# Performance work log

Measured on AMD Instinct MI355X. Metric: run time of the kernel, lower is better.

Reference implementation:

```python
import jax, jax.numpy as jnp
import numpy as np

NEG = jnp.float32(-9e15)
SLOPE = 0.2  # LeakyReLU negative slope used in LocalAggregator


def setup_inputs() -> dict:
    key = jax.random.key(0)
    k1, k2, k3, k4, k5, k6, k7 = jax.random.split(key, 7)
    B, N, D, V = 32, 200, 100, 50000
    stdv = 1.0 / np.sqrt(D)
    inputs = jax.random.randint(k1, (B, N), 0, V)
    adj = jax.random.randint(k2, (B, N, N), 0, 5).astype(jnp.int32)
    mask_item = jnp.ones((B, N), dtype=jnp.int32)
    emb = jax.random.uniform(k3, (V, D), jnp.float32, -stdv, stdv)
    a0 = jax.random.uniform(k4, (D, 1), jnp.float32, -stdv, stdv)
    a1 = jax.random.uniform(k5, (D, 1), jnp.float32, -stdv, stdv)
    a2 = jax.random.uniform(k6, (D, 1), jnp.float32, -stdv, stdv)
    a3 = jax.random.uniform(k7, (D, 1), jnp.float32, -stdv, stdv)
    return {"inputs": inputs, "adj": adj, "mask_item": mask_item,
            "emb": emb, "a0": a0, "a1": a1, "a2": a2, "a3": a3}


def reference(inputs, adj, mask_item, emb, a0, a1, a2, a3):
    # h: [B, N, D] session item embeddings
    h = emb[inputs]
    # e_k[b,i,j] = leaky_relu(sum_d h[b,i,d]*h[b,j,d]*a_k[d])
    # (equivalent to the original (h_i * h_j) @ a_k without the BxNxNxD blowup)
    def edge_score(a):
        s = jnp.einsum('bid,bjd->bij', h * a[:, 0][None, None, :], h)
        return jax.nn.leaky_relu(s, SLOPE)
    e0, e1, e2, e3 = edge_score(a0), edge_score(a1), edge_score(a2), edge_score(a3)
    alpha = jnp.where(adj == 1, e0, NEG)
    alpha = jnp.where(adj == 2, e1, alpha)
    alpha = jnp.where(adj == 3, e2, alpha)
    alpha = jnp.where(adj == 4, e3, alpha)
    alpha = jax.nn.softmax(alpha, axis=-1)  # [B, N, N]
    # weighted aggregation over neighbors; dropout_local is inactive in eval
    return jnp.einsum('bij,bjd->bid', alpha, h)
```

## Files before the change

### kernel.cpp

```cpp
#include <hip/hip_runtime.h>
#include <math.h>

#define NEGV  (-9e15f)
#define SLOPE 0.2f

typedef __fp16 f16;
typedef __fp16 f16x4 __attribute__((ext_vector_type(4)));
typedef __fp16 f16x8 __attribute__((ext_vector_type(8)));
typedef float  f32x4 __attribute__((ext_vector_type(4)));

#define ZERO8 {(f16)0.f,(f16)0.f,(f16)0.f,(f16)0.f,(f16)0.f,(f16)0.f,(f16)0.f,(f16)0.f}

__global__ __launch_bounds__(256, 2) void gat_v11_kernel(
    const int*   __restrict__ inputs,
    const int*   __restrict__ adj,
    const float* __restrict__ emb,
    const float* __restrict__ a0, const float* __restrict__ a1,
    const float* __restrict__ a2, const float* __restrict__ a3,
    float*       __restrict__ out)
{
    const int b    = blockIdx.x / 13;
    const int i0   = (blockIdx.x % 13) * 16;
    const int tid  = threadIdx.x;
    const int wave = tid >> 6, lane = tid & 63;
    const int lj   = lane & 15, quad = lane >> 4, rbase = quad * 4;

    __shared__ f16   HF[200][104];
    __shared__ f16   ST[200][24];
    __shared__ int   sidx[200];
    __shared__ float reds[16][4];

    int kvv[4][4];
    #pragma unroll
    for (int jt = 0; jt < 4; ++jt) {
        const int j = (wave + 4 * jt) * 16 + lj;
        #pragma unroll
        for (int reg = 0; reg < 4; ++reg) {
            const int gi = i0 + rbase + reg;
            kvv[jt][reg] = (j < 200 && gi < 200)
                         ? adj[(size_t)(b * 200 + gi) * 200 + j] : 0;
        }
    }

    for (int t = tid; t < 200; t += 256) sidx[t] = inputs[b * 200 + t];
    __syncthreads();

    const float* aks[4] = {a0, a1, a2, a3};
    const int irow = i0 + lj;
    const float* hp = emb + (size_t)sidx[(irow < 200) ? irow : 199] * 100;
    f16x8 afr[4][4];
    #pragma unroll
    for (int ks = 0; ks < 4; ++ks) {
        const int base = ks * 32 + quad * 8;
        const bool full = (base <= 88), part = (base == 96);
        float4 hx = {0.f,0.f,0.f,0.f}, hy = {0.f,0.f,0.f,0.f};
        if (full)      { hx = *(const float4*)(hp + base); hy = *(const float4*)(hp + base + 4); }
        else if (part) { hx = *(const float4*)(hp + 96); }
        #pragma unroll
        for (int kk = 0; kk < 4; ++kk) {
            f16x8 o = ZERO8;
            if (full) {
                const float4 ax = *(const float4*)(aks[kk] + base);
                const float4 ay = *(const float4*)(aks[kk] + base + 4);
                o[0]=(f16)(hx.x*ax.x); o[1]=(f16)(hx.y*ax.y);
                o[2]=(f16)(hx.z*ax.z); o[3]=(f16)(hx.w*ax.w);
                o[4]=(f16)(hy.x*ay.x); o[5]=(f16)(hy.y*ay.y);
                o[6]=(f16)(hy.z*ay.z); o[7]=(f16)(hy.w*ay.w);
            } else if (part) {
                const float4 ax = *(const float4*)(aks[kk] + 96);
                o[0]=(f16)(hx.x*ax.x); o[1]=(f16)(hx.y*ax.y);
                o[2]=(f16)(hx.z*ax.z); o[3]=(f16)(hx.w*ax.w);
            }
            afr[kk][ks] = o;
        }
    }

    if (tid < 200) {
        const float4* src = (const float4*)(emb + (size_t)sidx[tid] * 100);
        f16x8* dst = (f16x8*)&HF[tid][0];
        #pragma unroll
        for (int c = 0; c < 12; ++c) {
            const float4 x = src[2*c], y = src[2*c+1];
            f16x8 o;
            o[0]=(f16)x.x; o[1]=(f16)x.y; o[2]=(f16)x.z; o[3]=(f16)x.w;
            o[4]=(f16)y.x; o[5]=(f16)y.y; o[6]=(f16)y.z; o[7]=(f16)y.w;
            dst[c] = o;
        }
        const float4 x = src[24];
        f16x8 o = ZERO8;
        o[0]=(f16)x.x; o[1]=(f16)x.y; o[2]=(f16)x.z; o[3]=(f16)x.w;
        dst[12] = o;
    }
    __syncthreads();

    float sel[4][4];
    #pragma unroll
    for (int jt = 0; jt < 4; ++jt) {
        const int j  = (wave + 4*jt)*16 + lj;
        const int jr = (j < 200) ? j : 199;
        const f16x8 b0 = *(const f16x8*)&HF[jr][     quad*8];
        const f16x8 b1 = *(const f16x8*)&HF[jr][32 + quad*8];
        const f16x8 b2 = *(const f16x8*)&HF[jr][64 + quad*8];
        const f16x8 b3 = *(const f16x8*)&HF[jr][96];
        f32x4 acck[4];
        #pragma unroll
        for (int kk = 0; kk < 4; ++kk) {
            f32x4 c = {0.f,0.f,0.f,0.f};
            c = __builtin_amdgcn_mfma_f32_16x16x32_f16(afr[kk][0], b0, c, 0,0,0);
            c = __builtin_amdgcn_mfma_f32_16x16x32_f16(afr[kk][1], b1, c, 0,0,0);
            c = __builtin_amdgcn_mfma_f32_16x16x32_f16(afr[kk][2], b2, c, 0,0,0);
            c = __builtin_amdgcn_mfma_f32_16x16x32_f16(afr[kk][3], b3, c, 0,0,0);
            acck[kk] = c;
        }
        #pragma unroll
        for (int reg = 0; reg < 4; ++reg) {
            const int k = kvv[jt][reg];
            float s = NEGV;
            if (k >= 1 && k <= 4) {
                const float v = (k==1)?acck[0][reg]:(k==2)?acck[1][reg]
                              :(k==3)?acck[2][reg]:acck[3][reg];
                s = (v >= 0.f) ? v : SLOPE * v;
            }
            sel[jt][reg] = s;
        }
    }

    float e[4][4], lsum[4];
    #pragma unroll
    for (int reg = 0; reg < 4; ++reg) lsum[reg] = 0.f;
    #pragma unroll
    for (int jt = 0; jt < 4; ++jt)
        #pragma unroll
        for (int reg = 0; reg < 4; ++reg) {
            e[jt][reg] = __expf(sel[jt][reg]);
            lsum[reg] += e[jt][reg];
        }
    #pragma unroll
    for (int reg = 0; reg < 4; ++reg) {
        float s = lsum[reg];
        #pragma unroll
        for (int off = 1; off <= 8; off <<= 1) s += __shfl_xor(s, off, 16);
        if (lj == 0) reds[rbase + reg][wave] = s;
    }
    __syncthreads();
    float inv[4];
    #pragma unroll
    for (int reg = 0; reg < 4; ++reg) {
        const float* rr = reds[rbase + reg];
        inv[reg] = 1.0f / (rr[0] + rr[1] + rr[2] + rr[3]);
    }
    #pragma unroll
    for (int jt = 0; jt < 4; ++jt) {
        const int j = (wave + 4*jt)*16 + lj;
        if (j < 200) {
            f16x4 w;
            #pragma unroll
            for (int reg = 0; reg < 4; ++reg)
                w[reg] = (f16)(e[jt][reg] * inv[reg]);
            *(f16x4*)&ST[j][rbase] = w;
        }
    }
    __syncthreads();

    const int ig = tid & 7;
    const int dq = tid >> 3;
    f32x4 o[16];
    #pragma unroll
    for (int i = 0; i < 16; ++i) o[i] = (f32x4){0.f,0.f,0.f,0.f};
    if (dq < 25) {
        for (int jj = 0; jj < 25; ++jj) {
            const int j = ig * 25 + jj;
            const f16x8 w0 = *(const f16x8*)&ST[j][0];
            const f16x8 w1 = *(const f16x8*)&ST[j][8];
            const f16x4 hv = *(const f16x4*)&HF[j][dq * 4];
            const float h0 = (float)hv[0], h1 = (float)hv[1],
                        h2 = (float)hv[2], h3 = (float)hv[3];
            #pragma unroll
            for (int i = 0; i < 8; ++i) {
                const float w = (float)w0[i];
                o[i][0] += w * h0; o[i][1] += w * h1;
                o[i][2] += w * h2; o[i][3] += w * h3;
            }
            #pragma unroll
            for (int i = 0; i < 8; ++i) {
                const float w = (float)w1[i];
                o[8+i][0] += w * h0; o[8+i][1] += w * h1;
                o[8+i][2] += w * h2; o[8+i][3] += w * h3;
            }
        }
    }
    #pragma unroll
    for (int i = 0; i < 16; ++i)
        #pragma unroll
        for (int c = 0; c < 4; ++c)
            #pragma unroll
            for (int off = 1; off <= 4; off <<= 1)
                o[i][c] += __shfl_xor(o[i][c], off, 8);
    if (dq < 25) {
        #pragma unroll
        for (int ii = 0; ii < 2; ++ii) {
            const int i  = ig * 2 + ii;
            const int gi = i0 + i;
            if (gi < 200)
                ((f32x4*)out)[(size_t)(b * 200 + gi) * 25 + dq] = o[i];
        }
    }
}

extern "C" void kernel_launch(void* const* d_in, const int* in_sizes, int n_in,
                              void* d_out, int out_size, void* d_ws, size_t ws_size,
                              hipStream_t stream) {
    const int*   inputs = (const int*)  d_in[0];
    const int*   adj    = (const int*)  d_in[1];
    const float* emb    = (const float*)d_in[3];
    const float* a0     = (const float*)d_in[4];
    const float* a1     = (const float*)d_in[5];
    const float* a2     = (const float*)d_in[6];
    const float* a3     = (const float*)d_in[7];
    float*       out    = (float*)d_out;

    gat_v11_kernel<<<dim3(32 * 13), dim3(256), 0, stream>>>(inputs, adj, emb, a0, a1, a2, a3, out);
}
```

Baseline: 107.0 us.

## Pre-pack gathered embeddings to fp16 workspace in a separate kernel

Adds a pack kernel that gathers each session's embedding rows and converts them once to padded fp16 in workspace. The main kernel then copies its batch's fp16 rows into shared memory with coalesced vector loads, instead of each of the 13 blocks per batch re-gathering and re-converting fp32 rows. This cuts redundant global gather traffic and conversion work, at the cost of a second kernel launch and a workspace round trip. The A fragments are now built from fp16-rounded h instead of fp32 h, which slightly changes precision.

```diff
diff --git a/kernel.cpp b/kernel.cpp
--- a/kernel.cpp
+++ b/kernel.cpp
@@ -11,10 +11,31 @@
 
 #define ZERO8 {(f16)0.f,(f16)0.f,(f16)0.f,(f16)0.f,(f16)0.f,(f16)0.f,(f16)0.f,(f16)0.f}
 
-__global__ __launch_bounds__(256, 2) void gat_v11_kernel(
+__global__ __launch_bounds__(256) void pack_kernel(
     const int*   __restrict__ inputs,
+    const float* __restrict__ emb,
+    f16*         __restrict__ hw)
+{
+    const int t = blockIdx.x * 256 + threadIdx.x;
+    if (t >= 6400 * 13) return;
+    const int r = t / 13, c = t % 13;
+    const float* src = emb + (size_t)inputs[r] * 100 + c * 8;
+    f16x8 o = ZERO8;
+    if (c < 12) {
+        const float4 x = *(const float4*)src;
+        const float4 y = *(const float4*)(src + 4);
+        o[0]=(f16)x.x; o[1]=(f16)x.y; o[2]=(f16)x.z; o[3]=(f16)x.w;
+        o[4]=(f16)y.x; o[5]=(f16)y.y; o[6]=(f16)y.z; o[7]=(f16)y.w;
+    } else {
+        const float4 x = *(const float4*)src;
+        o[0]=(f16)x.x; o[1]=(f16)x.y; o[2]=(f16)x.z; o[3]=(f16)x.w;
+    }
+    *(f16x8*)(hw + (size_t)r * 104 + c * 8) = o;
+}
+
+__global__ __launch_bounds__(256, 2) void gat_v12_kernel(
     const int*   __restrict__ adj,
-    const float* __restrict__ emb,
+    const f16*   __restrict__ hw,
     const float* __restrict__ a0, const float* __restrict__ a1,
     const float* __restrict__ a2, const float* __restrict__ a3,
     float*       __restrict__ out)
@@ -27,7 +48,6 @@
 
     __shared__ f16   HF[200][104];
     __shared__ f16   ST[200][24];
-    __shared__ int   sidx[200];
     __shared__ float reds[16][4];
 
     int kvv[4][4];
@@ -42,54 +62,47 @@
         }
     }
 
-    for (int t = tid; t < 200; t += 256) sidx[t] = inputs[b * 200 + t];
-    __syncthreads();
-
     const float* aks[4] = {a0, a1, a2, a3};
     const int irow = i0 + lj;
-    const float* hp = emb + (size_t)sidx[(irow < 200) ? irow : 199] * 100;
+    const f16* hp16 = hw + (size_t)(b * 200 + ((irow < 200) ? irow : 199)) * 104;
     f16x8 afr[4][4];
     #pragma unroll
     for (int ks = 0; ks < 4; ++ks) {
         const int base = ks * 32 + quad * 8;
         const bool full = (base <= 88), part = (base == 96);
-        float4 hx = {0.f,0.f,0.f,0.f}, hy = {0.f,0.f,0.f,0.f};
-        if (full)      { hx = *(const float4*)(hp + base); hy = *(const float4*)(hp + base + 4); }
-        else if (part) { hx = *(const float4*)(hp + 96); }
-        #pragma unroll
-        for (int kk = 0; kk < 4; ++kk) {
-            f16x8 o = ZERO8;
-            if (full) {
+        #pragma unroll
+        for (int kk = 0; kk < 4; ++kk) afr[kk][ks] = (f16x8)ZERO8;
+        if (full) {
+            const f16x8 hx = *(const f16x8*)(hp16 + base);
+            #pragma unroll
+            for (int kk = 0; kk < 4; ++kk) {
                 const float4 ax = *(const float4*)(aks[kk] + base);
                 const float4 ay = *(const float4*)(aks[kk] + base + 4);
-                o[0]=(f16)(hx.x*ax.x); o[1]=(f16)(hx.y*ax.y);
-                o[2]=(f16)(hx.z*ax.z); o[3]=(f16)(hx.w*ax.w);
-                o[4]=(f16)(hy.x*ay.x); o[5]=(f16)(hy.y*ay.y);
-                o[6]=(f16)(hy.z*ay.z); o[7]=(f16)(hy.w*ay.w);
-            } else if (part) {
+                f16x8 o;
+                o[0]=(f16)((float)hx[0]*ax.x); o[1]=(f16)((float)hx[1]*ax.y);
+                o[2]=(f16)((float)hx[2]*ax.z); o[3]=(f16)((float)hx[3]*ax.w);
+                o[4]=(f16)((float)hx[4]*ay.x); o[5]=(f16)((float)hx[5]*ay.y);
+                o[6]=(f16)((float)hx[6]*ay.z); o[7]=(f16)((float)hx[7]*ay.w);
+                afr[kk][ks] = o;
+            }
+        } else if (part) {
+            const f16x8 hx = *(const f16x8*)(hp16 + 96);
+            #pragma unroll
+            for (int kk = 0; kk < 4; ++kk) {
                 const float4 ax = *(const float4*)(aks[kk] + 96);
-                o[0]=(f16)(hx.x*ax.x); o[1]=(f16)(hx.y*ax.y);
-                o[2]=(f16)(hx.z*ax.z); o[3]=(f16)(hx.w*ax.w);
-            }
-            afr[kk][ks] = o;
-        }
-    }
-
-    if (tid < 200) {
-        const float4* src = (const float4*)(emb + (size_t)sidx[tid] * 100);
-        f16x8* dst = (f16x8*)&HF[tid][0];
-        #pragma unroll
-        for (int c = 0; c < 12; ++c) {
-            const float4 x = src[2*c], y = src[2*c+1];
-            f16x8 o;
-            o[0]=(f16)x.x; o[1]=(f16)x.y; o[2]=(f16)x.z; o[3]=(f16)x.w;
-            o[4]=(f16)y.x; o[5]=(f16)y.y; o[6]=(f16)y.z; o[7]=(f16)y.w;
-            dst[c] = o;
-        }
-        const float4 x = src[24];
-        f16x8 o = ZERO8;
-        o[0]=(f16)x.x; o[1]=(f16)x.y; o[2]=(f16)x.z; o[3]=(f16)x.w;
-        dst[12] = o;
+                f16x8 o = ZERO8;
+                o[0]=(f16)((float)hx[0]*ax.x); o[1]=(f16)((float)hx[1]*ax.y);
+                o[2]=(f16)((float)hx[2]*ax.z); o[3]=(f16)((float)hx[3]*ax.w);
+                afr[kk][ks] = o;
+            }
+        }
+    }
+
+    {
+        const f16x8* src = (const f16x8*)(hw + (size_t)b * 200 * 104);
+        f16x8* dst = (f16x8*)&HF[0][0];
+        #pragma unroll
+        for (int t = tid; t < 200 * 13; t += 256) dst[t] = src[t];
     }
     __syncthreads();
 
@@ -218,6 +231,8 @@
     const float* a2     = (const float*)d_in[6];
     const float* a3     = (const float*)d_in[7];
     float*       out    = (float*)d_out;
-
-    gat_v11_kernel<<<dim3(32 * 13), dim3(256), 0, stream>>>(inputs, adj, emb, a0, a1, a2, a3, out);
+    f16*         hw     = (f16*)d_ws;
+
+    pack_kernel  <<<dim3(325),     dim3(256), 0, stream>>>(inputs, emb, hw);
+    gat_v12_kernel<<<dim3(32 * 13), dim3(256), 0, stream>>>(adj, hw, a0, a1, a2, a3, out);
 }
```

Measured after the change: 110.1 us. 2.9% more time.

## Compute aggregation stage with MFMA using transposed attention weights in LDS

Applied to the files above, without the earlier changes.

Replaces the scalar FMA aggregation (alpha @ H) with 16x16x32 f16 MFMA instructions. Attention weights are now stored row-major per query row (STi[16][232], zero-padded) so they load directly as A fragments. H columns are gathered element-wise from LDS as B fragments. HF row stride changes to 108 to reduce bank conflicts, which needs split f16x4 loads and stores. The intent is to remove the large scalar FMA loop and the shuffle reduction, at the cost of strided 2-byte LDS gathers and fewer active waves in the second column tile.

```diff
diff --git a/kernel.cpp b/kernel.cpp
--- a/kernel.cpp
+++ b/kernel.cpp
@@ -9,9 +9,19 @@
 typedef __fp16 f16x8 __attribute__((ext_vector_type(8)));
 typedef float  f32x4 __attribute__((ext_vector_type(4)));
 
+#define ZERO4 {(f16)0.f,(f16)0.f,(f16)0.f,(f16)0.f}
 #define ZERO8 {(f16)0.f,(f16)0.f,(f16)0.f,(f16)0.f,(f16)0.f,(f16)0.f,(f16)0.f,(f16)0.f}
 
-__global__ __launch_bounds__(256, 2) void gat_v11_kernel(
+__device__ __forceinline__ f16x8 ld8(const f16* p) {
+    const f16x4 a = *(const f16x4*)p;
+    const f16x4 c = *(const f16x4*)(p + 4);
+    f16x8 r;
+    r[0]=a[0]; r[1]=a[1]; r[2]=a[2]; r[3]=a[3];
+    r[4]=c[0]; r[5]=c[1]; r[6]=c[2]; r[7]=c[3];
+    return r;
+}
+
+__global__ __launch_bounds__(256, 2) void gat_v15_kernel(
     const int*   __restrict__ inputs,
     const int*   __restrict__ adj,
     const float* __restrict__ emb,
@@ -25,8 +35,8 @@
     const int wave = tid >> 6, lane = tid & 63;
     const int lj   = lane & 15, quad = lane >> 4, rbase = quad * 4;
 
-    __shared__ f16   HF[200][104];
-    __shared__ f16   ST[200][24];
+    __shared__ f16   HF[200][108];
+    __shared__ f16   STi[16][232];
     __shared__ int   sidx[200];
     __shared__ float reds[16][4];
 
@@ -43,6 +53,10 @@
     }
 
     for (int t = tid; t < 200; t += 256) sidx[t] = inputs[b * 200 + t];
+    if (tid < 64) {
+        const int i = tid >> 2, c = tid & 3;
+        *(f16x8*)&STi[i][200 + c * 8] = (f16x8)ZERO8;
+    }
     __syncthreads();
 
     const float* aks[4] = {a0, a1, a2, a3};
@@ -77,19 +91,21 @@
 
     if (tid < 200) {
         const float4* src = (const float4*)(emb + (size_t)sidx[tid] * 100);
-        f16x8* dst = (f16x8*)&HF[tid][0];
         #pragma unroll
         for (int c = 0; c < 12; ++c) {
             const float4 x = src[2*c], y = src[2*c+1];
-            f16x8 o;
-            o[0]=(f16)x.x; o[1]=(f16)x.y; o[2]=(f16)x.z; o[3]=(f16)x.w;
-            o[4]=(f16)y.x; o[5]=(f16)y.y; o[6]=(f16)y.z; o[7]=(f16)y.w;
-            dst[c] = o;
+            f16x4 lo, hi;
+            lo[0]=(f16)x.x; lo[1]=(f16)x.y; lo[2]=(f16)x.z; lo[3]=(f16)x.w;
+            hi[0]=(f16)y.x; hi[1]=(f16)y.y; hi[2]=(f16)y.z; hi[3]=(f16)y.w;
+            *(f16x4*)&HF[tid][c*8]     = lo;
+            *(f16x4*)&HF[tid][c*8 + 4] = hi;
         }
         const float4 x = src[24];
-        f16x8 o = ZERO8;
-        o[0]=(f16)x.x; o[1]=(f16)x.y; o[2]=(f16)x.z; o[3]=(f16)x.w;
-        dst[12] = o;
+        f16x4 lo;
+        lo[0]=(f16)x.x; lo[1]=(f16)x.y; lo[2]=(f16)x.z; lo[3]=(f16)x.w;
+        *(f16x4*)&HF[tid][96]  = lo;
+        *(f16x4*)&HF[tid][100] = (f16x4)ZERO4;
+        *(f16x4*)&HF[tid][104] = (f16x4)ZERO4;
     }
     __syncthreads();
 
@@ -98,10 +114,10 @@
     for (int jt = 0; jt < 4; ++jt) {
         const int j  = (wave + 4*jt)*16 + lj;
         const int jr = (j < 200) ? j : 199;
-        const f16x8 b0 = *(const f16x8*)&HF[jr][     quad*8];
-        const f16x8 b1 = *(const f16x8*)&HF[jr][32 + quad*8];
-        const f16x8 b2 = *(const f16x8*)&HF[jr][64 + quad*8];
-        const f16x8 b3 = *(const f16x8*)&HF[jr][96];
+        const f16x8 b0 = ld8(&HF[jr][     quad*8]);
+        const f16x8 b1 = ld8(&HF[jr][32 + quad*8]);
+        const f16x8 b2 = ld8(&HF[jr][64 + quad*8]);
+        const f16x8 b3 = ld8(&HF[jr][96]);
         f32x4 acck[4];
         #pragma unroll
         for (int kk = 0; kk < 4; ++kk) {
@@ -153,56 +169,39 @@
     for (int jt = 0; jt < 4; ++jt) {
         const int j = (wave + 4*jt)*16 + lj;
         if (j < 200) {
-            f16x4 w;
             #pragma unroll
             for (int reg = 0; reg < 4; ++reg)
-                w[reg] = (f16)(e[jt][reg] * inv[reg]);
-            *(f16x4*)&ST[j][rbase] = w;
-        }
-    }
-    __syncthreads();
-
-    const int ig = tid & 7;
-    const int dq = tid >> 3;
-    f32x4 o[16];
-    #pragma unroll
-    for (int i = 0; i < 16; ++i) o[i] = (f32x4){0.f,0.f,0.f,0.f};
-    if (dq < 25) {
-        for (int jj = 0; jj < 25; ++jj) {
-            const int j = ig * 25 + jj;
-            const f16x8 w0 = *(const f16x8*)&ST[j][0];
-            const f16x8 w1 = *(const f16x8*)&ST[j][8];
-            const f16x4 hv = *(const f16x4*)&HF[j][dq * 4];
-            const float h0 = (float)hv[0], h1 = (float)hv[1],
-                        h2 = (float)hv[2], h3 = (float)hv[3];
-            #pragma unroll
-            for (int i = 0; i < 8; ++i) {
-                const float w = (float)w0[i];
-                o[i][0] += w * h0; o[i][1] += w * h1;
-                o[i][2] += w * h2; o[i][3] += w * h3;
-            }
-            #pragma unroll
-            for (int i = 0; i < 8; ++i) {
-                const float w = (float)w1[i];
-                o[8+i][0] += w * h0; o[8+i][1] += w * h1;
-                o[8+i][2] += w * h2; o[8+i][3] += w * h3;
-            }
-        }
-    }
-    #pragma unroll
-    for (int i = 0; i < 16; ++i)
-        #pragma unroll
-        for (int c = 0; c < 4; ++c)
-            #pragma unroll
-            for (int off = 1; off <= 4; off <<= 1)
-                o[i][c] += __shfl_xor(o[i][c], off, 8);
-    if (dq < 25) {
-        #pragma unroll
-        for (int ii = 0; ii < 2; ++ii) {
-            const int i  = ig * 2 + ii;
-            const int gi = i0 + i;
-            if (gi < 200)
-                ((f32x4*)out)[(size_t)(b * 200 + gi) * 25 + dq] = o[i];
+                STi[rbase + reg][j] = (f16)(e[jt][reg] * inv[reg]);
+        }
+    }
+    __syncthreads();
+
+    f32x4 co0 = {0.f,0.f,0.f,0.f}, co1 = {0.f,0.f,0.f,0.f};
+    const int d0 = wave * 16 + lj;
+    const int d1 = (wave + 4) * 16 + lj;
+    const int d1r = (d1 < 107) ? d1 : 107;
+    #pragma unroll
+    for (int s = 0; s < 7; ++s) {
+        const f16x8 af = *(const f16x8*)&STi[lj][s*32 + quad*8];
+        f16x8 bg0, bg1;
+        #pragma unroll
+        for (int t2 = 0; t2 < 8; ++t2) {
+            const int j  = s*32 + quad*8 + t2;
+            const int jr = (j < 200) ? j : 199;
+            bg0[t2] = HF[jr][d0];
+            bg1[t2] = HF[jr][d1r];
+        }
+        co0 = __builtin_amdgcn_mfma_f32_16x16x32_f16(af, bg0, co0, 0,0,0);
+        if (wave < 3)
+            co1 = __builtin_amdgcn_mfma_f32_16x16x32_f16(af, bg1, co1, 0,0,0);
+    }
+    #pragma unroll
+    for (int reg = 0; reg < 4; ++reg) {
+        const int gi = i0 + rbase + reg;
+        if (gi < 200) {
+            float* orow = out + (size_t)(b * 200 + gi) * 100;
+            orow[d0] = co0[reg];
+            if (wave < 3 && d1 < 100) orow[d1] = co1[reg];
         }
     }
 }
@@ -219,5 +218,5 @@
     const float* a3     = (const float*)d_in[7];
     float*       out    = (float*)d_out;
 
-    gat_v11_kernel<<<dim3(32 * 13), dim3(256), 0, stream>>>(inputs, adj, emb, a0, a1, a2, a3, out);
+    gat_v15_kernel<<<dim3(32 * 13), dim3(256), 0, stream>>>(inputs, adj, emb, a0, a1, a2, a3, out);
 }
```

After: 94.69 us. -11.5%, faster.
